# Performance work log

Hardware: AMD Instinct MI355X
Metric: run time of the kernel (lower is better)

The kernel has to match this reference:

```python
import jax, jax.numpy as jnp
import numpy as np

D_MODEL = 1024
D_INNER = 2048   # expand_factor * d_model
D_STATE = 16
D_CONV = 4
DT_RANK = 64     # ceil(d_model / 16)
EPS = 1e-5


def setup_inputs() -> dict:
    key = jax.random.key(0)
    ks = jax.random.split(key, 10)
    B, L = 2, 1024
    w = lambda k, shape, s: (jax.random.normal(k, shape, jnp.float32) * s)
    A = jnp.tile(jnp.arange(1, D_STATE + 1, dtype=jnp.float32), (D_INNER, 1))
    return {
        "hidden_states": jax.random.normal(ks[0], (B, L, D_MODEL), jnp.float32),
        "norm_w": jnp.ones((D_MODEL,), jnp.float32),
        "norm_b": jnp.zeros((D_MODEL,), jnp.float32),
        "in_proj_w": w(ks[1], (D_MODEL, 2 * D_INNER), 0.02),
        "conv_w": w(ks[2], (D_INNER, D_CONV), 0.2),
        "conv_b": jnp.zeros((D_INNER,), jnp.float32),
        "x_proj_w": w(ks[3], (D_INNER, DT_RANK + 2 * D_STATE), 0.02),
        "dt_proj_w": w(ks[4], (DT_RANK, D_INNER), 0.1),
        "dt_proj_b": w(ks[5], (D_INNER,), 0.1),
        "A_log": jnp.log(A),
        "D_param": jnp.ones((D_INNER,), jnp.float32),
        "out_proj_w": w(ks[6], (D_INNER, D_MODEL), 0.02),
    }


def _causal_depthwise_conv(x, conv_w, conv_b):
    # x: [B, L, d_inner] -> causal depthwise conv, kernel size D_CONV
    B, L, C = x.shape
    xt = jnp.transpose(x, (0, 2, 1))                 # [B, C, L]
    xt = jnp.pad(xt, ((0, 0), (0, 0), (D_CONV - 1, 0)))  # left pad == torch pad+truncate
    k = conv_w[:, None, :]                            # [C, 1, K] (OIH, groups=C)
    y = jax.lax.conv_general_dilated(
        xt, k, window_strides=(1,), padding="VALID",
        dimension_numbers=("NCH", "OIH", "NCH"), feature_group_count=C)
    y = y + conv_b[None, :, None]
    return jnp.transpose(y, (0, 2, 1))                # [B, L, C]


def _selective_scan(u, delta, A, Bm, Cm, D_param):
    # u, delta: [B, L, d_inner]; A: [d_inner, d_state]; Bm, Cm: [B, L, d_state]
    dA = jnp.exp(delta[..., None] * A[None, None])            # [B,L,d,n]
    dBu = delta[..., None] * Bm[:, :, None, :] * u[..., None]  # [B,L,d,n]
    h0 = jnp.zeros((u.shape[0], u.shape[2], A.shape[1]), u.dtype)

    def step(h, inp):
        dA_t, dBu_t, c_t = inp          # [B,d,n], [B,d,n], [B,n]
        h = dA_t * h + dBu_t
        y = jnp.einsum("bdn,bn->bd", h, c_t)
        return h, y

    xs = (jnp.moveaxis(dA, 1, 0), jnp.moveaxis(dBu, 1, 0), jnp.moveaxis(Cm, 1, 0))
    _, ys = jax.lax.scan(step, h0, xs)   # ys: [L, B, d]
    y = jnp.moveaxis(ys, 0, 1)           # [B, L, d]
    return y + u * D_param[None, None]


def reference(hidden_states, norm_w, norm_b, in_proj_w, conv_w, conv_b,
              x_proj_w, dt_proj_w, dt_proj_b, A_log, D_param, out_proj_w):
    h = hidden_states
    mu = jnp.mean(h, axis=-1, keepdims=True)
    var = jnp.mean(jnp.square(h - mu), axis=-1, keepdims=True)
    h = (h - mu) * jax.lax.rsqrt(var + EPS) * norm_w + norm_b

    xz = h @ in_proj_w                       # [B,L,2*d_inner]
    x, z = jnp.split(xz, 2, axis=-1)
    x = _causal_depthwise_conv(x, conv_w, conv_b)
    x = jax.nn.silu(x)

    A = -jnp.exp(A_log)                      # [d_inner, d_state]
    xp = x @ x_proj_w                        # [B,L,dt_rank+2*d_state]
    dt_r = xp[..., :DT_RANK]
    Bm = xp[..., DT_RANK:DT_RANK + D_STATE]
    Cm = xp[..., DT_RANK + D_STATE:]
    delta = jax.nn.softplus(dt_r @ dt_proj_w + dt_proj_b)  # [B,L,d_inner]

    y = _selective_scan(x, delta, A, Bm, Cm, D_param)
    y = y * jax.nn.silu(z)
    return y @ out_proj_w
```

## Files before the change

kernel.cpp:

```cpp
#include <hip/hip_runtime.h>
#include <hip/hip_bf16.h>

#define D_MODEL 1024
#define D_INNER 2048
#define D_STATE 16
#define DT_RANK 64
#define NB 2
#define LSEQ 1024
#define NROWS (NB * LSEQ)
#define XPN 96
#define NC 32
#define CL 32

typedef __attribute__((ext_vector_type(8))) short bf16x8;
typedef __attribute__((ext_vector_type(4))) float f32x4;

__device__ __forceinline__ unsigned short f2bf(float x) {
    __hip_bfloat16 h = __float2bfloat16(x);
    return *reinterpret_cast<unsigned short*>(&h);
}

__device__ __forceinline__ size_t xzmap(size_t i) {
    return ((i >> 11) << 12) + (i & 2047);
}

__global__ __launch_bounds__(256) void ln_kernel(const float* __restrict__ x,
                                                 const float* __restrict__ w,
                                                 const float* __restrict__ bnorm,
                                                 unsigned short* __restrict__ outb) {
    int row = blockIdx.x;
    const float4* xr = (const float4*)(x + (size_t)row * D_MODEL);
    float4 v = xr[threadIdx.x];
    float s = v.x + v.y + v.z + v.w;
    float sq = v.x * v.x + v.y * v.y + v.z * v.z + v.w * v.w;
#pragma unroll
    for (int off = 32; off > 0; off >>= 1) {
        s += __shfl_down(s, off);
        sq += __shfl_down(sq, off);
    }
    __shared__ float ws[4], wq[4];
    __shared__ float smu, srstd;
    int wave = threadIdx.x >> 6;
    if ((threadIdx.x & 63) == 0) { ws[wave] = s; wq[wave] = sq; }
    __syncthreads();
    if (threadIdx.x == 0) {
        float ts = ws[0] + ws[1] + ws[2] + ws[3];
        float tq = wq[0] + wq[1] + wq[2] + wq[3];
        float mu = ts * (1.f / D_MODEL);
        float var = tq * (1.f / D_MODEL) - mu * mu;
        smu = mu;
        srstd = rsqrtf(var + 1e-5f);
    }
    __syncthreads();
    float mu = smu, rstd = srstd;
    float4 wv = ((const float4*)w)[threadIdx.x];
    float4 bv = ((const float4*)bnorm)[threadIdx.x];
    ushort4 pk;
    pk.x = f2bf((v.x - mu) * rstd * wv.x + bv.x);
    pk.y = f2bf((v.y - mu) * rstd * wv.y + bv.y);
    pk.z = f2bf((v.z - mu) * rstd * wv.z + bv.z);
    pk.w = f2bf((v.w - mu) * rstd * wv.w + bv.w);
    *(ushort4*)(outb + (size_t)row * D_MODEL + threadIdx.x * 4) = pk;
}

__global__ __launch_bounds__(256) void wcast_t(const float* __restrict__ W,
                                               unsigned short* __restrict__ Wt,
                                               int K, int Nreal, int Npad) {
    __shared__ float t[32][33];
    int tn = blockIdx.x * 32, tk = blockIdx.y * 32;
    for (int e = threadIdx.x; e < 1024; e += 256) {
        int r = e >> 5, c = e & 31;
        int n = tn + c;
        t[r][c] = (n < Nreal) ? W[(size_t)(tk + r) * Nreal + n] : 0.f;
    }
    __syncthreads();
    for (int e = threadIdx.x; e < 1024; e += 256) {
        int r = e >> 5, c = e & 31;
        Wt[(size_t)(tn + r) * K + tk + c] = f2bf(t[c][r]);
    }
}

template <int EPI>
__global__ __launch_bounds__(256) void gemm_bf16(const unsigned short* __restrict__ A,
                                                 const unsigned short* __restrict__ Bt,
                                                 const float* __restrict__ bias,
                                                 float* __restrict__ C,
                                                 int M, int K, int ldc, int Nreal) {
    __shared__ unsigned short As[128 * 32];
    __shared__ unsigned short Bs[128 * 32];
    int nwg = gridDim.x * gridDim.y;
    int orig = blockIdx.y * gridDim.x + blockIdx.x;
    int q = nwg >> 3, r = nwg & 7;
    int xcd = orig & 7, idx = orig >> 3;
    int newid = (xcd < r ? xcd * (q + 1) : r * (q + 1) + (xcd - r) * q) + idx;
    int bx = newid % gridDim.x, by = newid / gridDim.x;

    int tid = threadIdx.x;
    int lane = tid & 63;
    int wave = tid >> 6;
    int wr = (wave >> 1) * 64, wc = (wave & 1) * 64;
    int bm = by * 128, bn = bx * 128;
    int kchunk = K / gridDim.z;
    int kbeg = blockIdx.z * kchunk;

    f32x4 acc[4][4];
#pragma unroll
    for (int i = 0; i < 4; ++i)
#pragma unroll
        for (int j = 0; j < 4; ++j) acc[i][j] = (f32x4){0.f, 0.f, 0.f, 0.f};

    int r0 = tid >> 2;
    int c0 = (tid & 3) * 8;
    const unsigned short* a0 = A + (size_t)(bm + r0) * K + c0;
    const unsigned short* a1 = A + (size_t)(bm + 64 + r0) * K + c0;
    const unsigned short* b0 = Bt + (size_t)(bn + r0) * K + c0;
    const unsigned short* b1 = Bt + (size_t)(bn + 64 + r0) * K + c0;
    unsigned short* asw0 = As + (size_t)(tid & ~63) * 8;
    unsigned short* asw1 = As + 2048 + (size_t)(tid & ~63) * 8;
    unsigned short* bsw0 = Bs + (size_t)(tid & ~63) * 8;
    unsigned short* bsw1 = Bs + 2048 + (size_t)(tid & ~63) * 8;

    int ar = lane & 15;
    int ko = (lane >> 4) * 8;

    for (int k0 = kbeg; k0 < kbeg + kchunk; k0 += 32) {
        __syncthreads();
        __builtin_amdgcn_global_load_lds((const __attribute__((address_space(1))) void*)(a0 + k0),
                                         (__attribute__((address_space(3))) void*)asw0, 16, 0, 0);
        __builtin_amdgcn_global_load_lds((const __attribute__((address_space(1))) void*)(a1 + k0),
                                         (__attribute__((address_space(3))) void*)asw1, 16, 0, 0);
        __builtin_amdgcn_global_load_lds((const __attribute__((address_space(1))) void*)(b0 + k0),
                                         (__attribute__((address_space(3))) void*)bsw0, 16, 0, 0);
        __builtin_amdgcn_global_load_lds((const __attribute__((address_space(1))) void*)(b1 + k0),
                                         (__attribute__((address_space(3))) void*)bsw1, 16, 0, 0);
        __syncthreads();
        bf16x8 af[4], bfr[4];
#pragma unroll
        for (int i = 0; i < 4; ++i)
            af[i] = *(const bf16x8*)&As[(size_t)(wr + i * 16 + ar) * 32 + ko];
#pragma unroll
        for (int j = 0; j < 4; ++j)
            bfr[j] = *(const bf16x8*)&Bs[(size_t)(wc + j * 16 + ar) * 32 + ko];
#pragma unroll
        for (int i = 0; i < 4; ++i)
#pragma unroll
            for (int j = 0; j < 4; ++j)
                acc[i][j] = __builtin_amdgcn_mfma_f32_16x16x32_bf16(af[i], bfr[j], acc[i][j], 0, 0, 0);
    }

    int crow0 = bm + wr + (lane >> 4) * 4;
    int ccol0 = bn + wc + (lane & 15);
    size_t zoff = (size_t)blockIdx.z * (size_t)M * ldc;
#pragma unroll
    for (int i = 0; i < 4; ++i)
#pragma unroll
        for (int j = 0; j < 4; ++j) {
            int col = ccol0 + j * 16;
            if (col < Nreal) {
                float* cp = C + zoff + (size_t)(crow0 + i * 16) * ldc + col;
#pragma unroll
                for (int rr = 0; rr < 4; ++rr) {
                    float v = acc[i][j][rr];
                    if (EPI == 2) {
                        v += bias[col];
                        v = (v > 20.f) ? v : log1pf(__expf(v));
                    }
                    cp[(size_t)rr * ldc] = v;
                }
            }
        }
}

__global__ __launch_bounds__(256) void reduce_xp(const float* __restrict__ part,
                                                 float* __restrict__ xp,
                                                 unsigned short* __restrict__ dtr) {
    int t = blockIdx.x * 256 + threadIdx.x;
    float s = 0.f;
#pragma unroll
    for (int k = 0; k < 16; ++k) s += part[(size_t)k * (NROWS * XPN) + t];
    xp[t] = s;
    int row = t / 96, col = t - row * 96;
    if (col < 64) dtr[(size_t)row * 64 + col] = f2bf(s);
}

__global__ __launch_bounds__(256) void reduce_out(const float* __restrict__ part,
                                                  float* __restrict__ out) {
    int t = blockIdx.x * 256 + threadIdx.x;
    const float4* p = (const float4*)part;
    float4 a = p[t];
    float4 b = p[t + 524288];
    float4 c = p[t + 2 * 524288];
    float4 d = p[t + 3 * 524288];
    float4 o;
    o.x = a.x + b.x + c.x + d.x;
    o.y = a.y + b.y + c.y + d.y;
    o.z = a.z + b.z + c.z + d.z;
    o.w = a.w + b.w + c.w + d.w;
    ((float4*)out)[t] = o;
}

__global__ __launch_bounds__(256) void conv_silu_kernel(const float* __restrict__ xz,
                                                        const float* __restrict__ cw,
                                                        const float* __restrict__ cb,
                                                        float* __restrict__ out,
                                                        unsigned short* __restrict__ outb) {
    int gid = blockIdx.x * 256 + threadIdx.x;
    int d4 = (gid & 511) << 2;
    int bl = gid >> 9;
    int l = bl & (LSEQ - 1);
    const float* base = xz + (size_t)bl * (2 * D_INNER) + d4;
    float4 zr = make_float4(0.f, 0.f, 0.f, 0.f);
    float4 x0 = *(const float4*)base;
    float4 x1 = (l >= 1) ? *(const float4*)(base - 2 * D_INNER) : zr;
    float4 x2 = (l >= 2) ? *(const float4*)(base - 4 * D_INNER) : zr;
    float4 x3 = (l >= 3) ? *(const float4*)(base - 6 * D_INNER) : zr;
    float4 bias = *(const float4*)(cb + d4);
    float res[4];
    const float4* wv = (const float4*)(cw + (size_t)d4 * 4);
    float xs0[4] = {x0.x, x0.y, x0.z, x0.w};
    float xs1[4] = {x1.x, x1.y, x1.z, x1.w};
    float xs2[4] = {x2.x, x2.y, x2.z, x2.w};
    float xs3[4] = {x3.x, x3.y, x3.z, x3.w};
    float bs[4] = {bias.x, bias.y, bias.z, bias.w};
#pragma unroll
    for (int e = 0; e < 4; ++e) {
        float4 we = wv[e];
        float acc = bs[e];
        acc = fmaf(we.w, xs0[e], acc);
        acc = fmaf(we.z, xs1[e], acc);
        acc = fmaf(we.y, xs2[e], acc);
        acc = fmaf(we.x, xs3[e], acc);
        res[e] = acc / (1.f + __expf(-acc));
    }
    size_t oidx = (size_t)bl * D_INNER + d4;
    *(float4*)(out + oidx) = make_float4(res[0], res[1], res[2], res[3]);
    ushort4 ob;
    ob.x = f2bf(res[0]); ob.y = f2bf(res[1]); ob.z = f2bf(res[2]); ob.w = f2bf(res[3]);
    *(ushort4*)(outb + oidx) = ob;
}

__global__ __launch_bounds__(256) void scan_local(const float* __restrict__ xp,
                                                  const float* __restrict__ delta,
                                                  const float* __restrict__ xc,
                                                  const float* __restrict__ A_log,
                                                  float* __restrict__ xzh,
                                                  float* __restrict__ sdel) {
    int bc = blockIdx.x >> 3;
    int b = bc >> 5, c = bc & (NC - 1);
    int d = (blockIdx.x & 7) * 256 + threadIdx.x;
    int base_r = b * LSEQ + c * CL;
    __shared__ float Bs[CL * 16];
    for (int e = threadIdx.x; e < CL * 16; e += 256) {
        int l = e >> 4, n = e & 15;
        Bs[e] = xp[(size_t)(base_r + l) * XPN + DT_RANK + n];
    }
    __syncthreads();
    float Av[16];
    const float4* ap = (const float4*)(A_log + (size_t)d * 16);
#pragma unroll
    for (int qq = 0; qq < 4; ++qq) {
        float4 a = ap[qq];
        Av[4 * qq + 0] = -__expf(a.x); Av[4 * qq + 1] = -__expf(a.y);
        Av[4 * qq + 2] = -__expf(a.z); Av[4 * qq + 3] = -__expf(a.w);
    }
    float h[16] = {};
    float sd = 0.f;
    const float* dp = delta + (size_t)base_r * D_INNER + d;
    const float* up = xc + (size_t)base_r * D_INNER + d;
#pragma unroll 4
    for (int l = 0; l < CL; ++l) {
        float dv = dp[(size_t)l * D_INNER];
        float u = up[(size_t)l * D_INNER];
        float du = dv * u;
        sd += dv;
#pragma unroll
        for (int n = 0; n < 16; ++n) {
            float dA = __expf(dv * Av[n]);
            h[n] = fmaf(dA, h[n], du * Bs[l * 16 + n]);
        }
    }
    size_t hi = ((size_t)(c * NB + b) * D_INNER + d) * 16;
#pragma unroll
    for (int qq = 0; qq < 4; ++qq) {
        float4 v = make_float4(h[4 * qq], h[4 * qq + 1], h[4 * qq + 2], h[4 * qq + 3]);
        *(float4*)(xzh + xzmap(hi + 4 * qq)) = v;
    }
    sdel[(size_t)(c * NB + b) * D_INNER + d] = sd;
}

__global__ __launch_bounds__(256) void scan_combine(const float* __restrict__ A_log,
                                                    const float* __restrict__ sdel,
                                                    float* __restrict__ xzh) {
    int t = blockIdx.x * 256 + threadIdx.x;
    int n = t & 15, d = (t >> 4) & (D_INNER - 1), b = t >> 15;
    float Avn = -__expf(A_log[(size_t)d * 16 + n]);
    float h = 0.f;
#pragma unroll 4
    for (int c = 0; c < NC; ++c) {
        size_t base = (size_t)(c * NB + b) * D_INNER + d;
        float S = sdel[base];
        float* hp = xzh + xzmap(base * 16 + n);
        float tmp = *hp;
        *hp = h;
        h = fmaf(__expf(Avn * S), h, tmp);
    }
}

__global__ __launch_bounds__(256) void scan_final(const float* __restrict__ xp,
                                                  const float* __restrict__ dlt,
                                                  const float* __restrict__ xc,
                                                  const float* __restrict__ xz,
                                                  const float* __restrict__ A_log,
                                                  const float* __restrict__ Dp,
                                                  unsigned short* __restrict__ yb) {
    int bc = blockIdx.x >> 3;
    int b = bc >> 5, c = bc & (NC - 1);
    int d = (blockIdx.x & 7) * 256 + threadIdx.x;
    int base_r = b * LSEQ + c * CL;
    __shared__ float Bs[CL * 16], Cs[CL * 16];
    for (int e = threadIdx.x; e < CL * 16; e += 256) {
        int l = e >> 4, n = e & 15;
        Bs[e] = xp[(size_t)(base_r + l) * XPN + DT_RANK + n];
        Cs[e] = xp[(size_t)(base_r + l) * XPN + DT_RANK + 16 + n];
    }
    __syncthreads();
    float Av[16];
    const float4* ap = (const float4*)(A_log + (size_t)d * 16);
#pragma unroll
    for (int qq = 0; qq < 4; ++qq) {
        float4 a = ap[qq];
        Av[4 * qq + 0] = -__expf(a.x); Av[4 * qq + 1] = -__expf(a.y);
        Av[4 * qq + 2] = -__expf(a.z); Av[4 * qq + 3] = -__expf(a.w);
    }
    float h[16];
    size_t hi = ((size_t)(c * NB + b) * D_INNER + d) * 16;
#pragma unroll
    for (int qq = 0; qq < 4; ++qq) {
        float4 v = *(const float4*)(xz + xzmap(hi + 4 * qq));
        h[4 * qq] = v.x; h[4 * qq + 1] = v.y; h[4 * qq + 2] = v.z; h[4 * qq + 3] = v.w;
    }
    float Dv = Dp[d];
    const float* dyp = dlt + (size_t)base_r * D_INNER + d;
    const float* up = xc + (size_t)base_r * D_INNER + d;
    const float* zp = xz + (size_t)base_r * (2 * D_INNER) + D_INNER + d;
#pragma unroll 4
    for (int l = 0; l < CL; ++l) {
        float dv = dyp[(size_t)l * D_INNER];
        float u = up[(size_t)l * D_INNER];
        float du = dv * u;
        float acc = 0.f;
#pragma unroll
        for (int n = 0; n < 16; ++n) {
            float dA = __expf(dv * Av[n]);
            h[n] = fmaf(dA, h[n], du * Bs[l * 16 + n]);
            acc = fmaf(h[n], Cs[l * 16 + n], acc);
        }
        float yv = fmaf(u, Dv, acc);
        float zv = zp[(size_t)l * (2 * D_INNER)];
        float sz = zv / (1.f + __expf(-zv));
        yb[(size_t)(base_r + l) * D_INNER + d] = f2bf(yv * sz);
    }
}

extern "C" void kernel_launch(void* const* d_in, const int* in_sizes, int n_in,
                              void* d_out, int out_size, void* d_ws, size_t ws_size,
                              hipStream_t stream) {
    const float* hidden = (const float*)d_in[0];
    const float* norm_w = (const float*)d_in[1];
    const float* norm_b = (const float*)d_in[2];
    const float* in_proj_w = (const float*)d_in[3];
    const float* conv_w = (const float*)d_in[4];
    const float* conv_b = (const float*)d_in[5];
    const float* x_proj_w = (const float*)d_in[6];
    const float* dt_proj_w = (const float*)d_in[7];
    const float* dt_proj_b = (const float*)d_in[8];
    const float* A_log = (const float*)d_in[9];
    const float* D_param = (const float*)d_in[10];
    const float* out_proj_w = (const float*)d_in[11];
    float* out = (float*)d_out;

    float* wsf = (float*)d_ws;
    unsigned short* hbufb = (unsigned short*)wsf;
    float* xpbuf = wsf;
    float* sdelbuf = wsf + 196608;
    unsigned short* dtrb = (unsigned short*)(wsf + 327680);
    unsigned short* wDt = (unsigned short*)(wsf + 458752);
    unsigned short* wOt = (unsigned short*)wsf;
    float* xzbuf = wsf + 1048576;
    float* xcbuf = xzbuf + 8388608;
    unsigned short* xcb = (unsigned short*)(xcbuf + 4194304);
    unsigned short* yb = xcb;
    float* dltbuf = xcbuf + 4194304 + 2097152;
    unsigned short* wAt = (unsigned short*)dltbuf;
    float* xpart = dltbuf;
    unsigned short* wXt = (unsigned short*)(dltbuf + 3145728);

    wcast_t<<<dim3(4096 / 32, 1024 / 32), 256, 0, stream>>>(in_proj_w, wAt, 1024, 4096, 4096);
    wcast_t<<<dim3(128 / 32, 2048 / 32), 256, 0, stream>>>(x_proj_w, wXt, 2048, 96, 128);

    ln_kernel<<<NROWS, 256, 0, stream>>>(hidden, norm_w, norm_b, hbufb);

    gemm_bf16<0><<<dim3(4096 / 128, NROWS / 128, 1), 256, 0, stream>>>(
        hbufb, wAt, nullptr, xzbuf, NROWS, 1024, 4096, 4096);

    wcast_t<<<dim3(2048 / 32, 64 / 32), 256, 0, stream>>>(dt_proj_w, wDt, 64, 2048, 2048);

    conv_silu_kernel<<<(NROWS * D_INNER) / 1024, 256, 0, stream>>>(xzbuf, conv_w, conv_b, xcbuf, xcb);

    gemm_bf16<0><<<dim3(1, NROWS / 128, 16), 256, 0, stream>>>(
        xcb, wXt, nullptr, xpart, NROWS, 2048, XPN, XPN);

    reduce_xp<<<(NROWS * XPN) / 256, 256, 0, stream>>>(xpart, xpbuf, dtrb);

    gemm_bf16<2><<<dim3(D_INNER / 128, NROWS / 128, 1), 256, 0, stream>>>(
        dtrb, wDt, dt_proj_b, dltbuf, NROWS, 64, D_INNER, D_INNER);

    scan_local<<<NB * NC * (D_INNER / 256), 256, 0, stream>>>(
        xpbuf, dltbuf, xcbuf, A_log, xzbuf, sdelbuf);
    scan_combine<<<(NB * D_INNER * D_STATE) / 256, 256, 0, stream>>>(
        A_log, sdelbuf, xzbuf);
    scan_final<<<NB * NC * (D_INNER / 256), 256, 0, stream>>>(
        xpbuf, dltbuf, xcbuf, xzbuf, A_log, D_param, yb);

    wcast_t<<<dim3(1024 / 32, 2048 / 32), 256, 0, stream>>>(out_proj_w, wOt, 2048, 1024, 1024);

    gemm_bf16<0><<<dim3(1024 / 128, NROWS / 128, 4), 256, 0, stream>>>(
        yb, wOt, nullptr, xzbuf, NROWS, 2048, 1024, 1024);

    reduce_out<<<(NROWS * D_MODEL / 4) / 256, 256, 0, stream>>>(xzbuf, out);
}
```

Before: 199.9 us.

## Shrink intermediate buffers with bf16/fp16 storage across in_proj, conv, scan and out_proj

The in_proj GEMM now splits its output: the x half is stored as fp32 and the z gate half as bf16. The conv kernel no longer writes an fp32 copy of u, so the scan kernels read u and z as bf16. The scan state moves to a dedicated buffer. The out_proj split-K partials are stored as fp16 and reduced in fp32. All of this cuts global memory traffic across several kernels, at the cost of lower precision in the gate, the scan input and the partial sums.

```diff
diff --git a/kernel.cpp b/kernel.cpp
--- a/kernel.cpp
+++ b/kernel.cpp
@@ -19,9 +19,22 @@
     __hip_bfloat16 h = __float2bfloat16(x);
     return *reinterpret_cast<unsigned short*>(&h);
 }
-
-__device__ __forceinline__ size_t xzmap(size_t i) {
-    return ((i >> 11) << 12) + (i & 2047);
+__device__ __forceinline__ float bf2f(unsigned short u) {
+    unsigned int v = ((unsigned int)u) << 16;
+    float f;
+    __builtin_memcpy(&f, &v, 4);
+    return f;
+}
+__device__ __forceinline__ unsigned short f2h(float x) {
+    _Float16 h = (_Float16)x;
+    unsigned short u;
+    __builtin_memcpy(&u, &h, 2);
+    return u;
+}
+__device__ __forceinline__ float h2f(unsigned short u) {
+    _Float16 h;
+    __builtin_memcpy(&h, &u, 2);
+    return (float)h;
 }
 
 __global__ __launch_bounds__(256) void ln_kernel(const float* __restrict__ x,
@@ -85,6 +98,7 @@
                                                  const unsigned short* __restrict__ Bt,
                                                  const float* __restrict__ bias,
                                                  float* __restrict__ C,
+                                                 void* __restrict__ C2,
                                                  int M, int K, int ldc, int Nreal) {
     __shared__ unsigned short As[128 * 32];
     __shared__ unsigned short Bs[128 * 32];
@@ -156,17 +170,35 @@
 #pragma unroll
         for (int j = 0; j < 4; ++j) {
             int col = ccol0 + j * 16;
-            if (col < Nreal) {
-                float* cp = C + zoff + (size_t)(crow0 + i * 16) * ldc + col;
+            if (EPI == 0) {
+                if (col < Nreal) {
+                    float* cp = C + zoff + (size_t)(crow0 + i * 16) * ldc + col;
+#pragma unroll
+                    for (int rr = 0; rr < 4; ++rr) cp[(size_t)rr * ldc] = acc[i][j][rr];
+                }
+            } else if (EPI == 1) {
+                float bv = bias[col];
 #pragma unroll
                 for (int rr = 0; rr < 4; ++rr) {
-                    float v = acc[i][j][rr];
-                    if (EPI == 2) {
-                        v += bias[col];
-                        v = (v > 20.f) ? v : log1pf(__expf(v));
-                    }
-                    cp[(size_t)rr * ldc] = v;
+                    float v = acc[i][j][rr] + bv;
+                    v = (v > 20.f) ? v : log1pf(__expf(v));
+                    C[(size_t)(crow0 + i * 16 + rr) * ldc + col] = v;
                 }
+            } else if (EPI == 2) {
+                if (col < 2048) {
+#pragma unroll
+                    for (int rr = 0; rr < 4; ++rr)
+                        C[(size_t)(crow0 + i * 16 + rr) * 2048 + col] = acc[i][j][rr];
+                } else {
+                    unsigned short* cz = (unsigned short*)C2;
+#pragma unroll
+                    for (int rr = 0; rr < 4; ++rr)
+                        cz[(size_t)(crow0 + i * 16 + rr) * 2048 + (col - 2048)] = f2bf(acc[i][j][rr]);
+                }
+            } else {
+                unsigned short* cp = (unsigned short*)C2 + zoff + (size_t)(crow0 + i * 16) * ldc + col;
+#pragma unroll
+                for (int rr = 0; rr < 4; ++rr) cp[(size_t)rr * ldc] = f2h(acc[i][j][rr]);
             }
         }
 }
@@ -183,45 +215,45 @@
     if (col < 64) dtr[(size_t)row * 64 + col] = f2bf(s);
 }
 
-__global__ __launch_bounds__(256) void reduce_out(const float* __restrict__ part,
+__global__ __launch_bounds__(256) void reduce_out(const unsigned short* __restrict__ part,
                                                   float* __restrict__ out) {
     int t = blockIdx.x * 256 + threadIdx.x;
-    const float4* p = (const float4*)part;
-    float4 a = p[t];
-    float4 b = p[t + 524288];
-    float4 c = p[t + 2 * 524288];
-    float4 d = p[t + 3 * 524288];
+    const size_t stride = (size_t)NROWS * D_MODEL;
+    ushort4 p0 = ((const ushort4*)part)[t];
+    ushort4 p1 = ((const ushort4*)(part + stride))[t];
+    ushort4 p2 = ((const ushort4*)(part + 2 * stride))[t];
+    ushort4 p3 = ((const ushort4*)(part + 3 * stride))[t];
     float4 o;
-    o.x = a.x + b.x + c.x + d.x;
-    o.y = a.y + b.y + c.y + d.y;
-    o.z = a.z + b.z + c.z + d.z;
-    o.w = a.w + b.w + c.w + d.w;
+    o.x = h2f(p0.x) + h2f(p1.x) + h2f(p2.x) + h2f(p3.x);
+    o.y = h2f(p0.y) + h2f(p1.y) + h2f(p2.y) + h2f(p3.y);
+    o.z = h2f(p0.z) + h2f(p1.z) + h2f(p2.z) + h2f(p3.z);
+    o.w = h2f(p0.w) + h2f(p1.w) + h2f(p2.w) + h2f(p3.w);
     ((float4*)out)[t] = o;
 }
 
-__global__ __launch_bounds__(256) void conv_silu_kernel(const float* __restrict__ xz,
+__global__ __launch_bounds__(256) void conv_silu_kernel(const float* __restrict__ xx,
                                                         const float* __restrict__ cw,
                                                         const float* __restrict__ cb,
-                                                        float* __restrict__ out,
                                                         unsigned short* __restrict__ outb) {
     int gid = blockIdx.x * 256 + threadIdx.x;
     int d4 = (gid & 511) << 2;
     int bl = gid >> 9;
     int l = bl & (LSEQ - 1);
-    const float* base = xz + (size_t)bl * (2 * D_INNER) + d4;
+    const float* base = xx + (size_t)bl * D_INNER + d4;
     float4 zr = make_float4(0.f, 0.f, 0.f, 0.f);
     float4 x0 = *(const float4*)base;
-    float4 x1 = (l >= 1) ? *(const float4*)(base - 2 * D_INNER) : zr;
-    float4 x2 = (l >= 2) ? *(const float4*)(base - 4 * D_INNER) : zr;
-    float4 x3 = (l >= 3) ? *(const float4*)(base - 6 * D_INNER) : zr;
+    float4 x1 = (l >= 1) ? *(const float4*)(base - D_INNER) : zr;
+    float4 x2 = (l >= 2) ? *(const float4*)(base - 2 * D_INNER) : zr;
+    float4 x3 = (l >= 3) ? *(const float4*)(base - 3 * D_INNER) : zr;
     float4 bias = *(const float4*)(cb + d4);
-    float res[4];
     const float4* wv = (const float4*)(cw + (size_t)d4 * 4);
     float xs0[4] = {x0.x, x0.y, x0.z, x0.w};
     float xs1[4] = {x1.x, x1.y, x1.z, x1.w};
     float xs2[4] = {x2.x, x2.y, x2.z, x2.w};
     float xs3[4] = {x3.x, x3.y, x3.z, x3.w};
     float bs[4] = {bias.x, bias.y, bias.z, bias.w};
+    ushort4 ob;
+    unsigned short* obp = (unsigned short*)&ob;
 #pragma unroll
     for (int e = 0; e < 4; ++e) {
         float4 we = wv[e];
@@ -230,29 +262,25 @@
         acc = fmaf(we.z, xs1[e], acc);
         acc = fmaf(we.y, xs2[e], acc);
         acc = fmaf(we.x, xs3[e], acc);
-        res[e] = acc / (1.f + __expf(-acc));
-    }
-    size_t oidx = (size_t)bl * D_INNER + d4;
-    *(float4*)(out + oidx) = make_float4(res[0], res[1], res[2], res[3]);
-    ushort4 ob;
-    ob.x = f2bf(res[0]); ob.y = f2bf(res[1]); ob.z = f2bf(res[2]); ob.w = f2bf(res[3]);
-    *(ushort4*)(outb + oidx) = ob;
+        obp[e] = f2bf(acc / (1.f + __expf(-acc)));
+    }
+    *(ushort4*)(outb + (size_t)bl * D_INNER + d4) = ob;
 }
 
 __global__ __launch_bounds__(256) void scan_local(const float* __restrict__ xp,
                                                   const float* __restrict__ delta,
-                                                  const float* __restrict__ xc,
+                                                  const unsigned short* __restrict__ ub,
                                                   const float* __restrict__ A_log,
-                                                  float* __restrict__ xzh,
+                                                  float* __restrict__ hst,
                                                   float* __restrict__ sdel) {
     int bc = blockIdx.x >> 3;
     int b = bc >> 5, c = bc & (NC - 1);
     int d = (blockIdx.x & 7) * 256 + threadIdx.x;
     int base_r = b * LSEQ + c * CL;
-    __shared__ float Bs[CL * 16];
+    __shared__ float Bsm[CL * 16];
     for (int e = threadIdx.x; e < CL * 16; e += 256) {
         int l = e >> 4, n = e & 15;
-        Bs[e] = xp[(size_t)(base_r + l) * XPN + DT_RANK + n];
+        Bsm[e] = xp[(size_t)(base_r + l) * XPN + DT_RANK + n];
     }
     __syncthreads();
     float Av[16];
@@ -266,31 +294,31 @@
     float h[16] = {};
     float sd = 0.f;
     const float* dp = delta + (size_t)base_r * D_INNER + d;
-    const float* up = xc + (size_t)base_r * D_INNER + d;
+    const unsigned short* up = ub + (size_t)base_r * D_INNER + d;
 #pragma unroll 4
     for (int l = 0; l < CL; ++l) {
         float dv = dp[(size_t)l * D_INNER];
-        float u = up[(size_t)l * D_INNER];
+        float u = bf2f(up[(size_t)l * D_INNER]);
         float du = dv * u;
         sd += dv;
 #pragma unroll
         for (int n = 0; n < 16; ++n) {
             float dA = __expf(dv * Av[n]);
-            h[n] = fmaf(dA, h[n], du * Bs[l * 16 + n]);
+            h[n] = fmaf(dA, h[n], du * Bsm[l * 16 + n]);
         }
     }
     size_t hi = ((size_t)(c * NB + b) * D_INNER + d) * 16;
 #pragma unroll
     for (int qq = 0; qq < 4; ++qq) {
         float4 v = make_float4(h[4 * qq], h[4 * qq + 1], h[4 * qq + 2], h[4 * qq + 3]);
-        *(float4*)(xzh + xzmap(hi + 4 * qq)) = v;
+        *(float4*)(hst + hi + 4 * qq) = v;
     }
     sdel[(size_t)(c * NB + b) * D_INNER + d] = sd;
 }
 
 __global__ __launch_bounds__(256) void scan_combine(const float* __restrict__ A_log,
                                                     const float* __restrict__ sdel,
-                                                    float* __restrict__ xzh) {
+                                                    float* __restrict__ hst) {
     int t = blockIdx.x * 256 + threadIdx.x;
     int n = t & 15, d = (t >> 4) & (D_INNER - 1), b = t >> 15;
     float Avn = -__expf(A_log[(size_t)d * 16 + n]);
@@ -298,8 +326,8 @@
 #pragma unroll 4
     for (int c = 0; c < NC; ++c) {
         size_t base = (size_t)(c * NB + b) * D_INNER + d;
+        float* hp = hst + base * 16 + n;
         float S = sdel[base];
-        float* hp = xzh + xzmap(base * 16 + n);
         float tmp = *hp;
         *hp = h;
         h = fmaf(__expf(Avn * S), h, tmp);
@@ -308,8 +336,9 @@
 
 __global__ __launch_bounds__(256) void scan_final(const float* __restrict__ xp,
                                                   const float* __restrict__ dlt,
-                                                  const float* __restrict__ xc,
-                                                  const float* __restrict__ xz,
+                                                  const unsigned short* __restrict__ ub,
+                                                  const unsigned short* __restrict__ zb,
+                                                  const float* __restrict__ hst,
                                                   const float* __restrict__ A_log,
                                                   const float* __restrict__ Dp,
                                                   unsigned short* __restrict__ yb) {
@@ -317,11 +346,11 @@
     int b = bc >> 5, c = bc & (NC - 1);
     int d = (blockIdx.x & 7) * 256 + threadIdx.x;
     int base_r = b * LSEQ + c * CL;
-    __shared__ float Bs[CL * 16], Cs[CL * 16];
+    __shared__ float Bsm[CL * 16], Csm[CL * 16];
     for (int e = threadIdx.x; e < CL * 16; e += 256) {
         int l = e >> 4, n = e & 15;
-        Bs[e] = xp[(size_t)(base_r + l) * XPN + DT_RANK + n];
-        Cs[e] = xp[(size_t)(base_r + l) * XPN + DT_RANK + 16 + n];
+        Bsm[e] = xp[(size_t)(base_r + l) * XPN + DT_RANK + n];
+        Csm[e] = xp[(size_t)(base_r + l) * XPN + DT_RANK + 16 + n];
     }
     __syncthreads();
     float Av[16];
@@ -336,27 +365,27 @@
     size_t hi = ((size_t)(c * NB + b) * D_INNER + d) * 16;
 #pragma unroll
     for (int qq = 0; qq < 4; ++qq) {
-        float4 v = *(const float4*)(xz + xzmap(hi + 4 * qq));
+        float4 v = *(const float4*)(hst + hi + 4 * qq);
         h[4 * qq] = v.x; h[4 * qq + 1] = v.y; h[4 * qq + 2] = v.z; h[4 * qq + 3] = v.w;
     }
     float Dv = Dp[d];
     const float* dyp = dlt + (size_t)base_r * D_INNER + d;
-    const float* up = xc + (size_t)base_r * D_INNER + d;
-    const float* zp = xz + (size_t)base_r * (2 * D_INNER) + D_INNER + d;
+    const unsigned short* up = ub + (size_t)base_r * D_INNER + d;
+    const unsigned short* zp = zb + (size_t)base_r * D_INNER + d;
 #pragma unroll 4
     for (int l = 0; l < CL; ++l) {
         float dv = dyp[(size_t)l * D_INNER];
-        float u = up[(size_t)l * D_INNER];
+        float u = bf2f(up[(size_t)l * D_INNER]);
         float du = dv * u;
         float acc = 0.f;
 #pragma unroll
         for (int n = 0; n < 16; ++n) {
             float dA = __expf(dv * Av[n]);
-            h[n] = fmaf(dA, h[n], du * Bs[l * 16 + n]);
-            acc = fmaf(h[n], Cs[l * 16 + n], acc);
+            h[n] = fmaf(dA, h[n], du * Bsm[l * 16 + n]);
+            acc = fmaf(h[n], Csm[l * 16 + n], acc);
         }
         float yv = fmaf(u, Dv, acc);
-        float zv = zp[(size_t)l * (2 * D_INNER)];
+        float zv = bf2f(zp[(size_t)l * D_INNER]);
         float sz = zv / (1.f + __expf(-zv));
         yb[(size_t)(base_r + l) * D_INNER + d] = f2bf(yv * sz);
     }
@@ -386,46 +415,48 @@
     unsigned short* dtrb = (unsigned short*)(wsf + 327680);
     unsigned short* wDt = (unsigned short*)(wsf + 458752);
     unsigned short* wOt = (unsigned short*)wsf;
-    float* xzbuf = wsf + 1048576;
-    float* xcbuf = xzbuf + 8388608;
-    unsigned short* xcb = (unsigned short*)(xcbuf + 4194304);
+    float* xzx = wsf + 1048576;
+    unsigned short* xzz = (unsigned short*)(wsf + 5242880);
+    unsigned short* xcb = (unsigned short*)(wsf + 7340032);
     unsigned short* yb = xcb;
-    float* dltbuf = xcbuf + 4194304 + 2097152;
+    float* dltbuf = wsf + 9437184;
     unsigned short* wAt = (unsigned short*)dltbuf;
     float* xpart = dltbuf;
     unsigned short* wXt = (unsigned short*)(dltbuf + 3145728);
+    float* hst = xzx;
+    unsigned short* opart = (unsigned short*)xzx;
 
     wcast_t<<<dim3(4096 / 32, 1024 / 32), 256, 0, stream>>>(in_proj_w, wAt, 1024, 4096, 4096);
     wcast_t<<<dim3(128 / 32, 2048 / 32), 256, 0, stream>>>(x_proj_w, wXt, 2048, 96, 128);
 
     ln_kernel<<<NROWS, 256, 0, stream>>>(hidden, norm_w, norm_b, hbufb);
 
-    gemm_bf16<0><<<dim3(4096 / 128, NROWS / 128, 1), 256, 0, stream>>>(
-        hbufb, wAt, nullptr, xzbuf, NROWS, 1024, 4096, 4096);
+    gemm_bf16<2><<<dim3(4096 / 128, NROWS / 128, 1), 256, 0, stream>>>(
+        hbufb, wAt, nullptr, xzx, xzz, NROWS, 1024, 2048, 4096);
 
     wcast_t<<<dim3(2048 / 32, 64 / 32), 256, 0, stream>>>(dt_proj_w, wDt, 64, 2048, 2048);
 
-    conv_silu_kernel<<<(NROWS * D_INNER) / 1024, 256, 0, stream>>>(xzbuf, conv_w, conv_b, xcbuf, xcb);
+    conv_silu_kernel<<<(NROWS * D_INNER) / 1024, 256, 0, stream>>>(xzx, conv_w, conv_b, xcb);
 
     gemm_bf16<0><<<dim3(1, NROWS / 128, 16), 256, 0, stream>>>(
-        xcb, wXt, nullptr, xpart, NROWS, 2048, XPN, XPN);
+        xcb, wXt, nullptr, xpart, nullptr, NROWS, 2048, XPN, XPN);
 
     reduce_xp<<<(NROWS * XPN) / 256, 256, 0, stream>>>(xpart, xpbuf, dtrb);
 
-    gemm_bf16<2><<<dim3(D_INNER / 128, NROWS / 128, 1), 256, 0, stream>>>(
-        dtrb, wDt, dt_proj_b, dltbuf, NROWS, 64, D_INNER, D_INNER);
+    gemm_bf16<1><<<dim3(D_INNER / 128, NROWS / 128, 1), 256, 0, stream>>>(
+        dtrb, wDt, dt_proj_b, dltbuf, nullptr, NROWS, 64, D_INNER, D_INNER);
 
     scan_local<<<NB * NC * (D_INNER / 256), 256, 0, stream>>>(
-        xpbuf, dltbuf, xcbuf, A_log, xzbuf, sdelbuf);
+        xpbuf, dltbuf, xcb, A_log, hst, sdelbuf);
     scan_combine<<<(NB * D_INNER * D_STATE) / 256, 256, 0, stream>>>(
-        A_log, sdelbuf, xzbuf);
+        A_log, sdelbuf, hst);
     scan_final<<<NB * NC * (D_INNER / 256), 256, 0, stream>>>(
-        xpbuf, dltbuf, xcbuf, xzbuf, A_log, D_param, yb);
+        xpbuf, dltbuf, xcb, xzz, hst, A_log, D_param, yb);
 
     wcast_t<<<dim3(1024 / 32, 2048 / 32), 256, 0, stream>>>(out_proj_w, wOt, 2048, 1024, 1024);
 
-    gemm_bf16<0><<<dim3(1024 / 128, NROWS / 128, 4), 256, 0, stream>>>(
-        yb, wOt, nullptr, xzbuf, NROWS, 2048, 1024, 1024);
-
-    reduce_out<<<(NROWS * D_MODEL / 4) / 256, 256, 0, stream>>>(xzbuf, out);
-}
+    gemm_bf16<3><<<dim3(1024 / 128, NROWS / 128, 4), 256, 0, stream>>>(
+        yb, wOt, nullptr, nullptr, opart, NROWS, 2048, 1024, 1024);
+
+    reduce_out<<<(NROWS * D_MODEL / 4) / 256, 256, 0, stream>>>(opart, out);
+}
```

Measured after the change: 200.6 us. No clear change (+0.3%).
